# Optimization experiments

Hardware: AMD Instinct MI355X
Metric: run time of the kernel (lower is better)

Reference implementation:

```python
import jax, jax.numpy as jnp
import numpy as np

NEG = -1000000000.0

def _gat(x, adj_pos, W, a_src, a_dst):
    # x: [N,F], W: [H,F], a_src/a_dst: [1,H]
    h = x @ W.T                                          # [N,H]
    e = jax.nn.leaky_relu(h @ a_src.T + (h @ a_dst.T).T, 0.2)  # [N,N] additive attn
    e = jnp.where(adj_pos, e, NEG)
    alpha = jax.nn.softmax(e, axis=-1)
    return alpha @ h                                     # [N,H]

def setup_inputs() -> dict:
    key = jax.random.key(0)
    ks = jax.random.split(key, 24)
    N, F, Cf, C, H = 4096, 64, 10, 64, 128
    s = 0.05
    nrm = lambda k, shp: (jax.random.normal(k, shp, jnp.float32) * s)
    return dict(
        node_features=jax.random.normal(ks[0], (N, F), jnp.float32),
        candidate_features=jax.random.uniform(ks[1], (N, C, Cf), dtype=jnp.float32),
        adjacency=jax.random.randint(ks[2], (N, N), 0, 2).astype(jnp.int32),
        action_mask=jax.random.uniform(ks[3], (N, C), dtype=jnp.float32),
        W1=nrm(ks[4], (H, F)), a1s=nrm(ks[5], (1, H)), a1d=nrm(ks[6], (1, H)),
        W2=nrm(ks[7], (H, H)), a2s=nrm(ks[8], (1, H)), a2d=nrm(ks[9], (1, H)),
        ln_w=jnp.ones((H,), jnp.float32), ln_b=jnp.zeros((H,), jnp.float32),
        Wc1=nrm(ks[10], (H, Cf)), bc1=jnp.zeros((H,), jnp.float32),
        Wc2=nrm(ks[11], (H, H)), bc2=jnp.zeros((H,), jnp.float32),
        Wq=nrm(ks[12], (H, H)), bq=jnp.zeros((H,), jnp.float32),
        Ws1=nrm(ks[13], (H, 2 * H)), bs1=jnp.zeros((H,), jnp.float32),
        Ws2=nrm(ks[14], (1, H)), bs2=jnp.zeros((1,), jnp.float32),
    )

def reference(node_features, candidate_features, adjacency, action_mask,
              W1, a1s, a1d, W2, a2s, a2d, ln_w, ln_b,
              Wc1, bc1, Wc2, bc2, Wq, bq, Ws1, bs1, Ws2, bs2):
    gelu = lambda x: jax.nn.gelu(x, approximate=False)  # torch nn.GELU default (erf)
    adj_pos = adjacency > 0
    # two GAT layers with residual + LayerNorm
    h = jax.nn.relu(_gat(node_features, adj_pos, W1, a1s, a1d))      # [N,H]
    h = jax.nn.relu(_gat(h, adj_pos, W2, a2s, a2d)) + h
    mu = jnp.mean(h, axis=-1, keepdims=True)
    var = jnp.var(h, axis=-1, keepdims=True)
    h = (h - mu) * jax.lax.rsqrt(var + 1e-5) * ln_w + ln_b           # LayerNorm
    # candidate encoder
    cand = gelu(candidate_features @ Wc1.T + bc1)                    # [N,C,H]
    cand = gelu(cand @ Wc2.T + bc2)
    q = (h @ Wq.T + bq)[:, None, :]                                  # [N,1,H]
    fused = jnp.concatenate([q * cand, cand], axis=-1)               # [N,C,2H]
    logits = (gelu(fused @ Ws1.T + bs1) @ Ws2.T + bs2)[..., 0]       # [N,C]
    cf = candidate_features
    bias = (20.0 * cf[..., 0] + 4.0 * cf[..., 4] + 1.5 * cf[..., 5]
            + 1.5 * cf[..., 1] - 1.5 * cf[..., 2]
            + 1.2 * cf[..., 6] + 2.5 * cf[..., 7]
            + 1.6 * cf[..., 8] + 1.2 * cf[..., 9])
    logits = logits + bias
    # rows with no valid action: force action 0 valid
    no_valid = jnp.sum(action_mask, axis=-1) <= 0
    am = action_mask.at[:, 0].set(jnp.where(no_valid, 1.0, action_mask[:, 0]))
    return jnp.where(am > 0, logits, NEG)
```

## Files before the change

kernel.cpp:

```cpp
#include <hip/hip_runtime.h>
#include <hip/hip_bf16.h>
#include <math.h>

#define NN 4096
#define HD 128
#define NCAND 64
#define NCF 10
#define NSEG 16
#define NEGV (-1000000000.0f)

typedef __attribute__((ext_vector_type(8))) short short8_t;
typedef __attribute__((ext_vector_type(4))) float f32x4_t;

__device__ __forceinline__ short f2bf(float f) {
    union { __hip_bfloat16 h; short s; } v;
    v.h = __float2bfloat16(f);
    return v.s;
}
__device__ __forceinline__ float bf2f(short s) {
    union { unsigned u; float f; } v; v.u = ((unsigned)(unsigned short)s) << 16;
    return v.f;
}
__device__ __forceinline__ unsigned pk2(float a, float b) {
    union { __hip_bfloat162 h; unsigned u; } v;
    v.h = __float22bfloat162_rn(make_float2(a, b));
    return v.u;
}

__device__ __forceinline__ float gelu_f(float x) {
    float e = __builtin_amdgcn_exp2f(2.455466f * x);
    float r = __builtin_amdgcn_rcpf(e + 1.0f);
    return x - x * r;
}

__global__ __launch_bounds__(256) void prep_k(
    const int* __restrict__ adj, const float* __restrict__ Wc1,
    const float* __restrict__ Wc2, const float* __restrict__ Ws1,
    unsigned* __restrict__ adjb, short* __restrict__ Wc1b,
    short* __restrict__ Wc2b, short* __restrict__ Wfu)
{
    int tid = threadIdx.x;
    if (blockIdx.x < 2048) {
        long g = (long)blockIdx.x * 256 + tid;
        const int4* p = (const int4*)adj + g * 8;
        unsigned w = 0;
        #pragma unroll
        for (int e = 0; e < 8; ++e) {
            int4 v = p[e];
            w |= (unsigned)(v.x != 0) << (e*4 + 0);
            w |= (unsigned)(v.y != 0) << (e*4 + 1);
            w |= (unsigned)(v.z != 0) << (e*4 + 2);
            w |= (unsigned)(v.w != 0) << (e*4 + 3);
        }
        adjb[g] = w;
    } else {
        int g = (blockIdx.x - 2048) * 256 + tid;
        const int tot = 8 * 256;
        for (int e = g; e < 128*32; e += tot) {
            int t = e >> 5, k = e & 31;
            Wc1b[e] = (k < NCF) ? f2bf(Wc1[t*NCF + k]) : (short)0;
        }
        for (int e = g; e < 128*128; e += tot) {
            int h = e >> 7, pos = e & 127;
            int n = (pos >> 3) | ((pos & 7) << 4);
            Wc2b[e] = f2bf(Wc2[h*128 + n]);
        }
        for (int e = g; e < 128*256; e += tot) {
            int h = e >> 8, j = e & 255;
            int pos = j & 127;
            int n = (pos >> 3) | ((pos & 7) << 4);
            float v = (j < 128) ? Ws1[h*256 + 128 + n] : Ws1[h*256 + n];
            Wfu[e] = f2bf(v);
        }
    }
}

template<int K, int IN, int OUT>
__global__ __launch_bounds__(256) void gatin_k3(
    const float* __restrict__ in, const float* __restrict__ Wf,
    const float* __restrict__ nump, const float* __restrict__ denp,
    float* __restrict__ G1, const float* __restrict__ ln_w,
    const float* __restrict__ ln_b,
    const float* __restrict__ a_s, const float* __restrict__ a_d,
    float* __restrict__ sdv, short* __restrict__ Htb,
    const float* __restrict__ bias, float* __restrict__ outq)
{
    constexpr int AS = K + 4;
    __shared__ float in_s[16*AS];
    __shared__ float H_s[16*132];
    int tid = threadIdx.x;
    int n0 = blockIdx.x * 16;

    if (IN == 0) {
        constexpr int NV = 16*K/4;
        for (int idx = tid; idx < NV; idx += 256) {
            int row = idx / (K/4), c4 = idx - row*(K/4);
            *(float4*)&in_s[row*AS + c4*4] = *(const float4*)&in[(long)(n0+row)*K + c4*4];
        }
    } else {
        int row = tid >> 4, c8 = (tid & 15) * 8;
        float v[8];
        #pragma unroll
        for (int i = 0; i < 8; ++i) v[i] = 0.f;
        float den = 0.f;
        const float* npr = nump + (long)(n0 + row)*NSEG*HD + c8;
        const float* dpr = denp + (long)(n0 + row)*NSEG;
        #pragma unroll
        for (int s = 0; s < NSEG; ++s) {
            const float* np = npr + s*HD;
            float4 a0 = *(const float4*)np;
            float4 a1 = *(const float4*)(np + 4);
            v[0]+=a0.x; v[1]+=a0.y; v[2]+=a0.z; v[3]+=a0.w;
            v[4]+=a1.x; v[5]+=a1.y; v[6]+=a1.z; v[7]+=a1.w;
            den += dpr[s];
        }
        float rd = (den > 0.f) ? __builtin_amdgcn_rcpf(den) : 0.f;
        if (den > 0.f) rd = rd * (2.0f - den * rd);
        #pragma unroll
        for (int i = 0; i < 8; ++i) v[i] = fmaxf(v[i]*rd, 0.f);
        if (IN == 1) {
            float4 o0 = make_float4(v[0],v[1],v[2],v[3]);
            float4 o1 = make_float4(v[4],v[5],v[6],v[7]);
            *(float4*)&G1[(long)(n0+row)*HD + c8]     = o0;
            *(float4*)&G1[(long)(n0+row)*HD + c8 + 4] = o1;
        } else {
            const float* gp = G1 + (long)(n0+row)*HD + c8;
            float4 g0 = *(const float4*)gp;
            float4 g1 = *(const float4*)(gp + 4);
            v[0]+=g0.x; v[1]+=g0.y; v[2]+=g0.z; v[3]+=g0.w;
            v[4]+=g1.x; v[5]+=g1.y; v[6]+=g1.z; v[7]+=g1.w;
            float sm = 0.f, sq = 0.f;
            #pragma unroll
            for (int i = 0; i < 8; ++i) { sm += v[i]; sq += v[i]*v[i]; }
            sm += __shfl_xor(sm,1); sq += __shfl_xor(sq,1);
            sm += __shfl_xor(sm,2); sq += __shfl_xor(sq,2);
            sm += __shfl_xor(sm,4); sq += __shfl_xor(sq,4);
            sm += __shfl_xor(sm,8); sq += __shfl_xor(sq,8);
            float mu  = sm * (1.0f/128.0f);
            float var = sq * (1.0f/128.0f) - mu*mu;
            float nr  = rsqrtf(var + 1e-5f);
            float4 lw0 = *(const float4*)&ln_w[c8];
            float4 lw1 = *(const float4*)&ln_w[c8+4];
            float4 lb0 = *(const float4*)&ln_b[c8];
            float4 lb1 = *(const float4*)&ln_b[c8+4];
            v[0]=(v[0]-mu)*nr*lw0.x+lb0.x; v[1]=(v[1]-mu)*nr*lw0.y+lb0.y;
            v[2]=(v[2]-mu)*nr*lw0.z+lb0.z; v[3]=(v[3]-mu)*nr*lw0.w+lb0.w;
            v[4]=(v[4]-mu)*nr*lw1.x+lb1.x; v[5]=(v[5]-mu)*nr*lw1.y+lb1.y;
            v[6]=(v[6]-mu)*nr*lw1.z+lb1.z; v[7]=(v[7]-mu)*nr*lw1.w+lb1.w;
        }
        #pragma unroll
        for (int i = 0; i < 8; ++i) in_s[row*AS + c8 + i] = v[i];
    }
    __syncthreads();

    int w = tid >> 6, l = tid & 63, l15 = l & 15, qd = l >> 4;
    f32x4_t acc[2];
    acc[0] = (f32x4_t){0.f,0.f,0.f,0.f};
    acc[1] = (f32x4_t){0.f,0.f,0.f,0.f};
    #pragma unroll
    for (int kc = 0; kc < K/32; ++kc) {
        int k0 = kc*32 + qd*8;
        float4 x = *(const float4*)&in_s[l15*AS + k0];
        float4 y = *(const float4*)&in_s[l15*AS + k0 + 4];
        union { short8_t s; unsigned u[4]; } a;
        a.u[0]=pk2(x.x,x.y); a.u[1]=pk2(x.z,x.w);
        a.u[2]=pk2(y.x,y.y); a.u[3]=pk2(y.z,y.w);
        #pragma unroll
        for (int it = 0; it < 2; ++it) {
            int n = (w*2+it)*16 + l15;
            float4 w0 = *(const float4*)&Wf[(long)n*K + k0];
            float4 w1 = *(const float4*)&Wf[(long)n*K + k0 + 4];
            union { short8_t s; unsigned u[4]; } b;
            b.u[0]=pk2(w0.x,w0.y); b.u[1]=pk2(w0.z,w0.w);
            b.u[2]=pk2(w1.x,w1.y); b.u[3]=pk2(w1.z,w1.w);
            acc[it] = __builtin_amdgcn_mfma_f32_16x16x32_bf16(a.s, b.s, acc[it], 0,0,0);
        }
    }

    if (OUT == 1) {
        #pragma unroll
        for (int it = 0; it < 2; ++it) {
            int n = (w*2+it)*16 + l15;
            float bv = bias[n];
            #pragma unroll
            for (int r = 0; r < 4; ++r)
                outq[(long)(n0 + qd*4 + r)*HD + n] = acc[it][r] + bv;
        }
        return;
    }

    #pragma unroll
    for (int it = 0; it < 2; ++it)
        #pragma unroll
        for (int r = 0; r < 4; ++r)
            H_s[(qd*4+r)*132 + (w*2+it)*16 + l15] = acc[it][r];
    __syncthreads();
    {
        int row = tid >> 4, sg = tid & 15;
        int h0 = sg*8;
        float4 as0 = *(const float4*)&a_s[h0];
        float4 as1 = *(const float4*)&a_s[h0+4];
        float4 ad0 = *(const float4*)&a_d[h0];
        float4 ad1 = *(const float4*)&a_d[h0+4];
        float hv[8];
        #pragma unroll
        for (int e = 0; e < 8; ++e) hv[e] = H_s[row*132 + h0 + e];
        float sp = hv[0]*as0.x + hv[1]*as0.y + hv[2]*as0.z + hv[3]*as0.w
                 + hv[4]*as1.x + hv[5]*as1.y + hv[6]*as1.z + hv[7]*as1.w;
        float dp = hv[0]*ad0.x + hv[1]*ad0.y + hv[2]*ad0.z + hv[3]*ad0.w
                 + hv[4]*ad1.x + hv[5]*ad1.y + hv[6]*ad1.z + hv[7]*ad1.w;
        sp += __shfl_xor(sp,1); sp += __shfl_xor(sp,2);
        sp += __shfl_xor(sp,4); sp += __shfl_xor(sp,8);
        dp += __shfl_xor(dp,1); dp += __shfl_xor(dp,2);
        dp += __shfl_xor(dp,4); dp += __shfl_xor(dp,8);
        if (sg == 0) { sdv[n0+row] = sp; sdv[NN + n0 + row] = dp; }
    }
    {
        int h = tid & 127, pr = tid >> 7;
        unsigned u[4];
        #pragma unroll
        for (int c2 = 0; c2 < 4; ++c2)
            u[c2] = pk2(H_s[(pr*8 + 2*c2)*132 + h], H_s[(pr*8 + 2*c2 + 1)*132 + h]);
        *(uint4*)&Htb[(long)h*NN + n0 + pr*8] = make_uint4(u[0],u[1],u[2],u[3]);
    }
}

__global__ __launch_bounds__(256, 4) void agg_k5(
    const unsigned* __restrict__ adjb, const float* __restrict__ sdv,
    const short* __restrict__ Htb, float* __restrict__ num_part,
    float* __restrict__ den_part)
{
    __shared__ __align__(16) short Bs[128*72];
    __shared__ float dj_s[256];
    int tid = threadIdx.x;
    int i0 = blockIdx.x * 32;
    int seg = blockIdx.y;
    int w = tid >> 6, l = tid & 63, l15 = l & 15, qd = l >> 4;
    int mh = w >> 1, nh = w & 1;
    int arow = i0 + mh*16 + l15;
    float si = sdv[arow];
    const float C1 = 1.44269504f;
    const float C2 = 0.28853901f;

    dj_s[tid] = sdv[NN + seg*256 + tid];

    unsigned wbuf[8];
    {
        const uint4* ap = (const uint4*)&adjb[(long)arow*128 + seg*8];
        uint4 q0 = ap[0], q1 = ap[1];
        wbuf[0]=q0.x; wbuf[1]=q0.y; wbuf[2]=q0.z; wbuf[3]=q0.w;
        wbuf[4]=q1.x; wbuf[5]=q1.y; wbuf[6]=q1.z; wbuf[7]=q1.w;
    }

    int sh = tid >> 1, sj = (tid & 1) * 32;
    const short* srcb = Htb + (long)sh*NN + seg*256 + sj;

    f32x4_t acc[4];
    #pragma unroll
    for (int nt = 0; nt < 4; ++nt) acc[nt] = (f32x4_t){0.f,0.f,0.f,0.f};
    float den = 0.f;

    for (int c4 = 0; c4 < 4; ++c4) {
        __syncthreads();
        {
            const uint4* src = (const uint4*)(srcb + c4*64);
            uint4 v0 = src[0], v1 = src[1], v2 = src[2], v3 = src[3];
            uint4* dst = (uint4*)&Bs[sh*72 + sj];
            dst[0]=v0; dst[1]=v1; dst[2]=v2; dst[3]=v3;
        }
        __syncthreads();
        #pragma unroll
        for (int kc = 0; kc < 2; ++kc) {
            int jl = c4*64 + kc*32 + qd*8;
            float4 da = *(const float4*)&dj_s[jl];
            float4 db = *(const float4*)&dj_s[jl+4];
            unsigned byte_ = (wbuf[c4*2+kc] >> (qd*8)) & 0xffu;
            float dv[8] = {da.x,da.y,da.z,da.w,db.x,db.y,db.z,db.w};
            float v[8];
            #pragma unroll
            for (int e = 0; e < 8; ++e) {
                float z = si + dv[e];
                float k = (z > 0.f) ? C1 : C2;
                float wv = __builtin_amdgcn_exp2f(z * k);
                v[e] = ((byte_ >> e) & 1u) ? wv : 0.f;
                den += v[e];
            }
            union { short8_t s; unsigned u[4]; } a;
            a.u[0]=pk2(v[0],v[1]); a.u[1]=pk2(v[2],v[3]);
            a.u[2]=pk2(v[4],v[5]); a.u[3]=pk2(v[6],v[7]);
            int kb = kc*32 + qd*8;
            #pragma unroll
            for (int nt = 0; nt < 4; ++nt) {
                short8_t b = *(const short8_t*)&Bs[(nh*64 + nt*16 + l15)*72 + kb];
                acc[nt] = __builtin_amdgcn_mfma_f32_16x16x32_bf16(a.s, b, acc[nt], 0,0,0);
            }
        }
    }
    den += __shfl_xor(den, 16); den += __shfl_xor(den, 32);
    if (qd == 0 && nh == 0) den_part[(long)arow*NSEG + seg] = den;
    #pragma unroll
    for (int nt = 0; nt < 4; ++nt)
        #pragma unroll
        for (int r = 0; r < 4; ++r)
            num_part[((long)(i0 + mh*16 + qd*4 + r)*NSEG + seg)*HD
                     + nh*64 + nt*16 + l15] = acc[nt][r];
}

__device__ __forceinline__ short8_t mulq2(short8_t c, float4 qa, float4 qb) {
    union { short8_t s; unsigned u[4]; } r;
    r.u[0] = pk2(bf2f(c[0])*qa.x, bf2f(c[1])*qa.y);
    r.u[1] = pk2(bf2f(c[2])*qa.z, bf2f(c[3])*qa.w);
    r.u[2] = pk2(bf2f(c[4])*qb.x, bf2f(c[5])*qb.y);
    r.u[3] = pk2(bf2f(c[6])*qb.z, bf2f(c[7])*qb.w);
    return r.s;
}

__global__ __launch_bounds__(256, 4) void cand_k8(
    const float* __restrict__ cf, const float* __restrict__ am,
    const float* __restrict__ Qb,
    const short* __restrict__ Wc1b, const short* __restrict__ Wc2b,
    const short* __restrict__ Wfu,
    const float* __restrict__ bc1, const float* __restrict__ bc2,
    const float* __restrict__ bs1, const float* __restrict__ Ws2,
    const float* __restrict__ bs2, float* __restrict__ out)
{
    __shared__ __align__(16) short cand_s[128*136];
    __shared__ float bias_s[128];
    __shared__ __align__(16) float q_s[2][128];
    __shared__ float red_s[128*4];
    __shared__ float noval_s[2];
    int tid = threadIdx.x;
    long r0 = (long)blockIdx.x * 128;
    int w = tid >> 6, l = tid & 63, l15 = l & 15, qd = l >> 4;

    {
        float amv = am[r0 + (long)(w >> 1)*64 + l];
        float tot = amv;
        #pragma unroll
        for (int off = 32; off > 0; off >>= 1) tot += __shfl_xor(tot, off);
        if ((w & 1) == 0 && l == 0) noval_s[w >> 1] = (tot <= 0.f) ? 1.f : 0.f;
    }

    {
        int nd = tid >> 7, n = tid & 127;
        float qv = Qb[((r0 >> 6) + nd)*HD + n];
        int pos = ((n & 15) << 3) | (n >> 4);
        q_s[nd][pos] = qv;
    }

    {
        short8_t fa[2];
        #pragma unroll
        for (int im = 0; im < 2; ++im) {
            long row = r0 + (w*2+im)*16 + l15;
            union { short8_t s; unsigned u[4]; } a;
            float bp = 0.f;
            if (qd == 0) {
                float4 x = *(const float4*)&cf[row*10];
                float4 y = *(const float4*)&cf[row*10+4];
                a.u[0]=pk2(x.x,x.y); a.u[1]=pk2(x.z,x.w);
                a.u[2]=pk2(y.x,y.y); a.u[3]=pk2(y.z,y.w);
                bp = 20.0f*x.x + 1.5f*x.y - 1.5f*x.z + 4.0f*y.x
                   + 1.5f*y.y + 1.2f*y.z + 2.5f*y.w;
            } else if (qd == 1) {
                float2 x = *(const float2*)&cf[row*10+8];
                a.u[0]=pk2(x.x,x.y); a.u[1]=0; a.u[2]=0; a.u[3]=0;
                bp = 1.6f*x.x + 1.2f*x.y;
            } else { a.u[0]=a.u[1]=a.u[2]=a.u[3]=0; }
            bp += __shfl_xor(bp, 16);
            if (qd == 0) bias_s[(w*2+im)*16 + l15] = bp;
            fa[im] = a.s;
        }
        f32x4_t acc1[2][8];
        #pragma unroll
        for (int im = 0; im < 2; ++im)
            #pragma unroll
            for (int nt = 0; nt < 8; ++nt) acc1[im][nt] = (f32x4_t){0.f,0.f,0.f,0.f};
        #pragma unroll
        for (int nt = 0; nt < 8; ++nt) {
            short8_t b = *(const short8_t*)&Wc1b[(nt*16 + l15)*32 + qd*8];
            acc1[0][nt] = __builtin_amdgcn_mfma_f32_16x16x32_bf16(fa[0], b, acc1[0][nt], 0,0,0);
            acc1[1][nt] = __builtin_amdgcn_mfma_f32_16x16x32_bf16(fa[1], b, acc1[1][nt], 0,0,0);
        }
        float bv[8];
        #pragma unroll
        for (int nt = 0; nt < 8; ++nt) bv[nt] = bc1[nt*16 + l15];
        #pragma unroll
        for (int im = 0; im < 2; ++im)
            #pragma unroll
            for (int r = 0; r < 4; ++r) {
                unsigned u[4];
                #pragma unroll
                for (int ph = 0; ph < 4; ++ph) {
                    float g0 = gelu_f(acc1[im][2*ph][r]   + bv[2*ph]);
                    float g1 = gelu_f(acc1[im][2*ph+1][r] + bv[2*ph+1]);
                    u[ph] = pk2(g0, g1);
                }
                int m = (w*2+im)*16 + qd*4 + r;
                *(uint4*)&cand_s[m*136 + l15*8] = make_uint4(u[0],u[1],u[2],u[3]);
            }
    }
    __syncthreads();

    f32x4_t acc[8][2];
    #pragma unroll
    for (int mt = 0; mt < 8; ++mt) {
        acc[mt][0] = (f32x4_t){0.f,0.f,0.f,0.f};
        acc[mt][1] = (f32x4_t){0.f,0.f,0.f,0.f};
    }
    #pragma unroll
    for (int kc = 0; kc < 4; ++kc) {
        int kpos = kc*32 + qd*8;
        short8_t a[8];
        #pragma unroll
        for (int mt = 0; mt < 8; ++mt)
            a[mt] = *(const short8_t*)&cand_s[(mt*16 + l15)*136 + kpos];
        short8_t b0 = *(const short8_t*)&Wc2b[((w*2+0)*16 + l15)*128 + kpos];
        short8_t b1 = *(const short8_t*)&Wc2b[((w*2+1)*16 + l15)*128 + kpos];
        #pragma unroll
        for (int mt = 0; mt < 8; ++mt) {
            acc[mt][0] = __builtin_amdgcn_mfma_f32_16x16x32_bf16(a[mt], b0, acc[mt][0], 0,0,0);
            acc[mt][1] = __builtin_amdgcn_mfma_f32_16x16x32_bf16(a[mt], b1, acc[mt][1], 0,0,0);
        }
    }
    __syncthreads();

    {
        float bv0 = bc2[w*32 + l15];
        float bv1 = bc2[w*32 + 16 + l15];
        #pragma unroll
        for (int mt = 0; mt < 8; ++mt)
            #pragma unroll
            for (int r = 0; r < 4; ++r) {
                float g0 = gelu_f(acc[mt][0][r] + bv0);
                float g1 = gelu_f(acc[mt][1][r] + bv1);
                int m = mt*16 + qd*4 + r;
                *(unsigned*)&cand_s[m*136 + l15*8 + w*2] = pk2(g0, g1);
            }
    }
    __syncthreads();

    #pragma unroll
    for (int mt = 0; mt < 8; ++mt) {
        acc[mt][0] = (f32x4_t){0.f,0.f,0.f,0.f};
        acc[mt][1] = (f32x4_t){0.f,0.f,0.f,0.f};
    }
    #pragma unroll
    for (int kc = 0; kc < 4; ++kc) {
        int kpos = kc*32 + qd*8;
        short8_t a[8];
        #pragma unroll
        for (int mt = 0; mt < 8; ++mt)
            a[mt] = *(const short8_t*)&cand_s[(mt*16 + l15)*136 + kpos];
        short8_t b00 = *(const short8_t*)&Wfu[((w*2+0)*16 + l15)*256 + kpos];
        short8_t b10 = *(const short8_t*)&Wfu[((w*2+1)*16 + l15)*256 + kpos];
        short8_t b01 = *(const short8_t*)&Wfu[((w*2+0)*16 + l15)*256 + 128 + kpos];
        short8_t b11 = *(const short8_t*)&Wfu[((w*2+1)*16 + l15)*256 + 128 + kpos];
        float4 qa0 = *(const float4*)&q_s[0][kpos];
        float4 qb0 = *(const float4*)&q_s[0][kpos+4];
        float4 qa1 = *(const float4*)&q_s[1][kpos];
        float4 qb1 = *(const float4*)&q_s[1][kpos+4];
        short8_t b01q0 = mulq2(b01, qa0, qb0);
        short8_t b11q0 = mulq2(b11, qa0, qb0);
        short8_t b01q1 = mulq2(b01, qa1, qb1);
        short8_t b11q1 = mulq2(b11, qa1, qb1);
        #pragma unroll
        for (int mt = 0; mt < 8; ++mt) {
            short8_t bq0 = (mt < 4) ? b01q0 : b01q1;
            short8_t bq1 = (mt < 4) ? b11q0 : b11q1;
            acc[mt][0] = __builtin_amdgcn_mfma_f32_16x16x32_bf16(a[mt], b00, acc[mt][0], 0,0,0);
            acc[mt][1] = __builtin_amdgcn_mfma_f32_16x16x32_bf16(a[mt], b10, acc[mt][1], 0,0,0);
            acc[mt][0] = __builtin_amdgcn_mfma_f32_16x16x32_bf16(a[mt], bq0, acc[mt][0], 0,0,0);
            acc[mt][1] = __builtin_amdgcn_mfma_f32_16x16x32_bf16(a[mt], bq1, acc[mt][1], 0,0,0);
        }
    }

    {
        float bs1v0 = bs1[w*32 + l15],      bs1v1 = bs1[w*32 + 16 + l15];
        float ws2v0 = Ws2[w*32 + l15],      ws2v1 = Ws2[w*32 + 16 + l15];
        #pragma unroll
        for (int mt = 0; mt < 8; ++mt)
            #pragma unroll
            for (int r = 0; r < 4; ++r) {
                float p = gelu_f(acc[mt][0][r] + bs1v0) * ws2v0
                        + gelu_f(acc[mt][1][r] + bs1v1) * ws2v1;
                p += __shfl_xor(p,1); p += __shfl_xor(p,2);
                p += __shfl_xor(p,4); p += __shfl_xor(p,8);
                if (l15 == 0)
                    red_s[(mt*16 + qd*4 + r)*4 + w] = p;
            }
    }
    __syncthreads();

    if (tid < 128) {
        int m = tid;
        float lg = red_s[m*4] + red_s[m*4+1] + red_s[m*4+2] + red_s[m*4+3]
                 + bs2[0] + bias_s[m];
        float mk = am[r0 + m];
        if ((m & 63) == 0 && noval_s[m >> 6] > 0.f) mk = 1.0f;
        out[r0 + m] = (mk > 0.f) ? lg : NEGV;
    }
}

extern "C" void kernel_launch(void* const* d_in, const int* in_sizes, int n_in,
                              void* d_out, int out_size, void* d_ws, size_t ws_size,
                              hipStream_t stream)
{
    const float* X   = (const float*)d_in[0];
    const float* CF  = (const float*)d_in[1];
    const int*   ADJ = (const int*)d_in[2];
    const float* AM  = (const float*)d_in[3];
    const float* W1  = (const float*)d_in[4];
    const float* A1S = (const float*)d_in[5];
    const float* A1D = (const float*)d_in[6];
    const float* W2  = (const float*)d_in[7];
    const float* A2S = (const float*)d_in[8];
    const float* A2D = (const float*)d_in[9];
    const float* LNW = (const float*)d_in[10];
    const float* LNB = (const float*)d_in[11];
    const float* WC1 = (const float*)d_in[12];
    const float* BC1 = (const float*)d_in[13];
    const float* WC2 = (const float*)d_in[14];
    const float* BC2 = (const float*)d_in[15];
    const float* WQ  = (const float*)d_in[16];
    const float* BQ  = (const float*)d_in[17];
    const float* WS1 = (const float*)d_in[18];
    const float* BS1 = (const float*)d_in[19];
    const float* WS2 = (const float*)d_in[20];
    const float* BS2 = (const float*)d_in[21];
    float* OUT = (float*)d_out;

    float* ws = (float*)d_ws;
    float*    G1   = ws;
    float*    Qb   = ws + 524288;
    float*    sdv  = ws + 1048576;
    float*    denp = ws + 1056768;
    short*    Htb  = (short*)(ws + 1122304);
    unsigned* adjb = (unsigned*)(ws + 1384448);
    short*    Wc1b = (short*)(ws + 1908736);
    short*    Wc2b = (short*)(ws + 1910784);
    short*    Wfu  = (short*)(ws + 1918976);
    float*    nump = ws + 1935360;

    prep_k<<<2056, 256, 0, stream>>>(ADJ, WC1, WC2, WS1, adjb, Wc1b, Wc2b, Wfu);

    gatin_k3<64, 0, 0><<<256, 256, 0, stream>>>(
        X, W1, nullptr, nullptr, nullptr, nullptr, nullptr,
        A1S, A1D, sdv, Htb, nullptr, nullptr);
    agg_k5<<<dim3(128, NSEG), 256, 0, stream>>>(adjb, sdv, Htb, nump, denp);

    gatin_k3<128, 1, 0><<<256, 256, 0, stream>>>(
        nullptr, W2, nump, denp, G1, nullptr, nullptr,
        A2S, A2D, sdv, Htb, nullptr, nullptr);
    agg_k5<<<dim3(128, NSEG), 256, 0, stream>>>(adjb, sdv, Htb, nump, denp);

    gatin_k3<128, 2, 1><<<256, 256, 0, stream>>>(
        nullptr, WQ, nump, denp, G1, LNW, LNB,
        nullptr, nullptr, nullptr, nullptr, BQ, Qb);

    cand_k8<<<2048, 256, 0, stream>>>(CF, AM, Qb, Wc1b, Wc2b, Wfu,
                                      BC1, BC2, BS1, WS2, BS2, OUT);
}
```

Baseline: 270.3 us.

## Fuse first GAT projection into prep kernel and fold LN+Q projection into candidate kernel

Merges the layer-1 GAT input projection into the preprocessing launch as extra blocks, and moves the final aggregation, residual, LayerNorm and Wq projection into the candidate kernel, which each block now computes for its two nodes. This cuts two kernel launches and the Qb round trip through global memory. In exchange, each candidate block now does a scalar fp32 128x128 matvec and reads 16 partial segments per node. The serialized prologue before the main candidate MFMA work may add latency.

```diff
diff --git a/kernel.cpp b/kernel.cpp
--- a/kernel.cpp
+++ b/kernel.cpp
@@ -33,27 +33,36 @@
     return x - x * r;
 }
 
-__global__ __launch_bounds__(256) void prep_k(
+__global__ __launch_bounds__(256) void prep_gatin_k(
     const int* __restrict__ adj, const float* __restrict__ Wc1,
     const float* __restrict__ Wc2, const float* __restrict__ Ws1,
     unsigned* __restrict__ adjb, short* __restrict__ Wc1b,
-    short* __restrict__ Wc2b, short* __restrict__ Wfu)
+    short* __restrict__ Wc2b, short* __restrict__ Wfu,
+    const float* __restrict__ X, const float* __restrict__ W1,
+    const float* __restrict__ a_s, const float* __restrict__ a_d,
+    float* __restrict__ sdv, short* __restrict__ Htb)
 {
+    constexpr int K = 64, AS = 68;
+    __shared__ float in_s[16*AS];
+    __shared__ float H_s[16*132];
     int tid = threadIdx.x;
+
     if (blockIdx.x < 2048) {
         long g = (long)blockIdx.x * 256 + tid;
         const int4* p = (const int4*)adj + g * 8;
-        unsigned w = 0;
+        unsigned wd = 0;
         #pragma unroll
         for (int e = 0; e < 8; ++e) {
             int4 v = p[e];
-            w |= (unsigned)(v.x != 0) << (e*4 + 0);
-            w |= (unsigned)(v.y != 0) << (e*4 + 1);
-            w |= (unsigned)(v.z != 0) << (e*4 + 2);
-            w |= (unsigned)(v.w != 0) << (e*4 + 3);
-        }
-        adjb[g] = w;
-    } else {
+            wd |= (unsigned)(v.x != 0) << (e*4 + 0);
+            wd |= (unsigned)(v.y != 0) << (e*4 + 1);
+            wd |= (unsigned)(v.z != 0) << (e*4 + 2);
+            wd |= (unsigned)(v.w != 0) << (e*4 + 3);
+        }
+        adjb[g] = wd;
+        return;
+    }
+    if (blockIdx.x < 2056) {
         int g = (blockIdx.x - 2048) * 256 + tid;
         const int tot = 8 * 256;
         for (int e = g; e < 128*32; e += tot) {
@@ -72,6 +81,75 @@
             float v = (j < 128) ? Ws1[h*256 + 128 + n] : Ws1[h*256 + n];
             Wfu[e] = f2bf(v);
         }
+        return;
+    }
+
+    int n0 = (blockIdx.x - 2056) * 16;
+    {
+        constexpr int NV = 16*K/4;
+        for (int idx = tid; idx < NV; idx += 256) {
+            int row = idx / (K/4), c4 = idx - row*(K/4);
+            *(float4*)&in_s[row*AS + c4*4] = *(const float4*)&X[(long)(n0+row)*K + c4*4];
+        }
+    }
+    __syncthreads();
+
+    int w = tid >> 6, l = tid & 63, l15 = l & 15, qd = l >> 4;
+    f32x4_t acc[2];
+    acc[0] = (f32x4_t){0.f,0.f,0.f,0.f};
+    acc[1] = (f32x4_t){0.f,0.f,0.f,0.f};
+    #pragma unroll
+    for (int kc = 0; kc < K/32; ++kc) {
+        int k0 = kc*32 + qd*8;
+        float4 x = *(const float4*)&in_s[l15*AS + k0];
+        float4 y = *(const float4*)&in_s[l15*AS + k0 + 4];
+        union { short8_t s; unsigned u[4]; } a;
+        a.u[0]=pk2(x.x,x.y); a.u[1]=pk2(x.z,x.w);
+        a.u[2]=pk2(y.x,y.y); a.u[3]=pk2(y.z,y.w);
+        #pragma unroll
+        for (int it = 0; it < 2; ++it) {
+            int n = (w*2+it)*16 + l15;
+            float4 w0 = *(const float4*)&W1[(long)n*K + k0];
+            float4 w1 = *(const float4*)&W1[(long)n*K + k0 + 4];
+            union { short8_t s; unsigned u[4]; } b;
+            b.u[0]=pk2(w0.x,w0.y); b.u[1]=pk2(w0.z,w0.w);
+            b.u[2]=pk2(w1.x,w1.y); b.u[3]=pk2(w1.z,w1.w);
+            acc[it] = __builtin_amdgcn_mfma_f32_16x16x32_bf16(a.s, b.s, acc[it], 0,0,0);
+        }
+    }
+    #pragma unroll
+    for (int it = 0; it < 2; ++it)
+        #pragma unroll
+        for (int r = 0; r < 4; ++r)
+            H_s[(qd*4+r)*132 + (w*2+it)*16 + l15] = acc[it][r];
+    __syncthreads();
+    {
+        int row = tid >> 4, sg = tid & 15;
+        int h0 = sg*8;
+        float4 as0 = *(const float4*)&a_s[h0];
+        float4 as1 = *(const float4*)&a_s[h0+4];
+        float4 ad0 = *(const float4*)&a_d[h0];
+        float4 ad1 = *(const float4*)&a_d[h0+4];
+        float hv[8];
+        #pragma unroll
+        for (int e = 0; e < 8; ++e) hv[e] = H_s[row*132 + h0 + e];
+        float sp = hv[0]*as0.x + hv[1]*as0.y + hv[2]*as0.z + hv[3]*as0.w
+                 + hv[4]*as1.x + hv[5]*as1.y + hv[6]*as1.z + hv[7]*as1.w;
+        float dp = hv[0]*ad0.x + hv[1]*ad0.y + hv[2]*ad0.z + hv[3]*ad0.w
+                 + hv[4]*ad1.x + hv[5]*ad1.y + hv[6]*ad1.z + hv[7]*ad1.w;
+        sp += __shfl_xor(sp,1); sp += __shfl_xor(sp,2);
+        sp += __shfl_xor(sp,4); sp += __shfl_xor(sp,8);
+        dp += __shfl_xor(dp,1); dp += __shfl_xor(dp,2);
+        dp += __shfl_xor(dp,4); dp += __shfl_xor(dp,8);
+        if (sg == 0) { sdv[n0+row] = sp; sdv[NN + n0 + row] = dp; }
+    }
+    {
+        int h = tid & 127, pr = tid >> 7;
+        unsigned u[4];
+        #pragma unroll
+        for (int c2 = 0; c2 < 4; ++c2)
+            u[c2] = pk2(H_s[(pr*8 + 2*c2)*132 + h], H_s[(pr*8 + 2*c2 + 1)*132 + h]);
+        *(uint4*)&Htb[(long)h*NN + n0 + pr*8] = make_uint4(u[0],u[1],u[2],u[3]);
     }
 }
 
@@ -123,30 +201,6 @@
             float4 o1 = make_float4(v[4],v[5],v[6],v[7]);
             *(float4*)&G1[(long)(n0+row)*HD + c8]     = o0;
             *(float4*)&G1[(long)(n0+row)*HD + c8 + 4] = o1;
-        } else {
-            const float* gp = G1 + (long)(n0+row)*HD + c8;
-            float4 g0 = *(const float4*)gp;
-            float4 g1 = *(const float4*)(gp + 4);
-            v[0]+=g0.x; v[1]+=g0.y; v[2]+=g0.z; v[3]+=g0.w;
-            v[4]+=g1.x; v[5]+=g1.y; v[6]+=g1.z; v[7]+=g1.w;
-            float sm = 0.f, sq = 0.f;
-            #pragma unroll
-            for (int i = 0; i < 8; ++i) { sm += v[i]; sq += v[i]*v[i]; }
-            sm += __shfl_xor(sm,1); sq += __shfl_xor(sq,1);
-            sm += __shfl_xor(sm,2); sq += __shfl_xor(sq,2);
-            sm += __shfl_xor(sm,4); sq += __shfl_xor(sq,4);
-            sm += __shfl_xor(sm,8); sq += __shfl_xor(sq,8);
-            float mu  = sm * (1.0f/128.0f);
-            float var = sq * (1.0f/128.0f) - mu*mu;
-            float nr  = rsqrtf(var + 1e-5f);
-            float4 lw0 = *(const float4*)&ln_w[c8];
-            float4 lw1 = *(const float4*)&ln_w[c8+4];
-            float4 lb0 = *(const float4*)&ln_b[c8];
-            float4 lb1 = *(const float4*)&ln_b[c8+4];
-            v[0]=(v[0]-mu)*nr*lw0.x+lb0.x; v[1]=(v[1]-mu)*nr*lw0.y+lb0.y;
-            v[2]=(v[2]-mu)*nr*lw0.z+lb0.z; v[3]=(v[3]-mu)*nr*lw0.w+lb0.w;
-            v[4]=(v[4]-mu)*nr*lw1.x+lb1.x; v[5]=(v[5]-mu)*nr*lw1.y+lb1.y;
-            v[6]=(v[6]-mu)*nr*lw1.z+lb1.z; v[7]=(v[7]-mu)*nr*lw1.w+lb1.w;
         }
         #pragma unroll
         for (int i = 0; i < 8; ++i) in_s[row*AS + c8 + i] = v[i];
@@ -175,18 +229,6 @@
             b.u[2]=pk2(w1.x,w1.y); b.u[3]=pk2(w1.z,w1.w);
             acc[it] = __builtin_amdgcn_mfma_f32_16x16x32_bf16(a.s, b.s, acc[it], 0,0,0);
         }
-    }
-
-    if (OUT == 1) {
-        #pragma unroll
-        for (int it = 0; it < 2; ++it) {
-            int n = (w*2+it)*16 + l15;
-            float bv = bias[n];
-            #pragma unroll
-            for (int r = 0; r < 4; ++r)
-                outq[(long)(n0 + qd*4 + r)*HD + n] = acc[it][r] + bv;
-        }
-        return;
     }
 
     #pragma unroll
@@ -315,9 +357,12 @@
     return r.s;
 }
 
-__global__ __launch_bounds__(256, 4) void cand_k8(
+__global__ __launch_bounds__(256, 4) void cand_k9(
     const float* __restrict__ cf, const float* __restrict__ am,
-    const float* __restrict__ Qb,
+    const float* __restrict__ nump, const float* __restrict__ denp,
+    const float* __restrict__ G1, const float* __restrict__ ln_w,
+    const float* __restrict__ ln_b, const float* __restrict__ Wq,
+    const float* __restrict__ bq,
     const short* __restrict__ Wc1b, const short* __restrict__ Wc2b,
     const short* __restrict__ Wfu,
     const float* __restrict__ bc1, const float* __restrict__ bc2,
@@ -329,6 +374,7 @@
     __shared__ __align__(16) float q_s[2][128];
     __shared__ float red_s[128*4];
     __shared__ float noval_s[2];
+    __shared__ float hln_s[2][128];
     int tid = threadIdx.x;
     long r0 = (long)blockIdx.x * 128;
     int w = tid >> 6, l = tid & 63, l15 = l & 15, qd = l >> 4;
@@ -341,11 +387,50 @@
         if ((w & 1) == 0 && l == 0) noval_s[w >> 1] = (tot <= 0.f) ? 1.f : 0.f;
     }
 
-    {
-        int nd = tid >> 7, n = tid & 127;
-        float qv = Qb[((r0 >> 6) + nd)*HD + n];
+    if (w < 2) {
+        int node = (int)(r0 >> 6) + w;
+        float v0 = 0.f, v1 = 0.f, den = 0.f;
+        const float* np = nump + (long)node*NSEG*HD;
+        const float* dp = denp + (long)node*NSEG;
+        #pragma unroll
+        for (int s = 0; s < NSEG; ++s) {
+            v0 += np[s*HD + l];
+            v1 += np[s*HD + l + 64];
+            den += dp[s];
+        }
+        float rd = (den > 0.f) ? __builtin_amdgcn_rcpf(den) : 0.f;
+        if (den > 0.f) rd = rd * (2.0f - den * rd);
+        v0 = fmaxf(v0*rd, 0.f) + G1[(long)node*HD + l];
+        v1 = fmaxf(v1*rd, 0.f) + G1[(long)node*HD + l + 64];
+        float sm = v0 + v1, sq = v0*v0 + v1*v1;
+        #pragma unroll
+        for (int off = 32; off > 0; off >>= 1) {
+            sm += __shfl_xor(sm, off);
+            sq += __shfl_xor(sq, off);
+        }
+        float mu  = sm * (1.0f/128.0f);
+        float var = sq * (1.0f/128.0f) - mu*mu;
+        float nr  = rsqrtf(var + 1e-5f);
+        hln_s[w][l]      = (v0 - mu)*nr*ln_w[l]      + ln_b[l];
+        hln_s[w][l + 64] = (v1 - mu)*nr*ln_w[l + 64] + ln_b[l + 64];
+    }
+    __syncthreads();
+
+    if (tid < 128) {
+        int n = tid;
+        const float* wq = Wq + (long)n*HD;
+        const float* h0 = hln_s[0];
+        const float* h1 = hln_s[1];
+        float a0 = bq[n], a1 = a0;
+        #pragma unroll 8
+        for (int k = 0; k < 128; k += 4) {
+            float4 wv = *(const float4*)&wq[k];
+            a0 += h0[k]*wv.x + h0[k+1]*wv.y + h0[k+2]*wv.z + h0[k+3]*wv.w;
+            a1 += h1[k]*wv.x + h1[k+1]*wv.y + h1[k+2]*wv.z + h1[k+3]*wv.w;
+        }
         int pos = ((n & 15) << 3) | (n >> 4);
-        q_s[nd][pos] = qv;
+        q_s[0][pos] = a0;
+        q_s[1][pos] = a1;
     }
 
     {
@@ -532,32 +617,24 @@
 
     float* ws = (float*)d_ws;
     float*    G1   = ws;
-    float*    Qb   = ws + 524288;
-    float*    sdv  = ws + 1048576;
-    float*    denp = ws + 1056768;
-    short*    Htb  = (short*)(ws + 1122304);
-    unsigned* adjb = (unsigned*)(ws + 1384448);
-    short*    Wc1b = (short*)(ws + 1908736);
-    short*    Wc2b = (short*)(ws + 1910784);
-    short*    Wfu  = (short*)(ws + 1918976);
-    float*    nump = ws + 1935360;
-
-    prep_k<<<2056, 256, 0, stream>>>(ADJ, WC1, WC2, WS1, adjb, Wc1b, Wc2b, Wfu);
-
-    gatin_k3<64, 0, 0><<<256, 256, 0, stream>>>(
-        X, W1, nullptr, nullptr, nullptr, nullptr, nullptr,
-        A1S, A1D, sdv, Htb, nullptr, nullptr);
+    float*    sdv  = ws + 524288;
+    float*    denp = ws + 532480;
+    short*    Htb  = (short*)(ws + 598016);
+    unsigned* adjb = (unsigned*)(ws + 860160);
+    short*    Wc1b = (short*)(ws + 1384448);
+    short*    Wc2b = (short*)(ws + 1386496);
+    short*    Wfu  = (short*)(ws + 1394688);
+    float*    nump = ws + 1411072;
+
+    prep_gatin_k<<<2312, 256, 0, stream>>>(ADJ, WC1, WC2, WS1,
+                                           adjb, Wc1b, Wc2b, Wfu,
+                                           X, W1, A1S, A1D, sdv, Htb);
     agg_k5<<<dim3(128, NSEG), 256, 0, stream>>>(adjb, sdv, Htb, nump, denp);
-
     gatin_k3<128, 1, 0><<<256, 256, 0, stream>>>(
         nullptr, W2, nump, denp, G1, nullptr, nullptr,
         A2S, A2D, sdv, Htb, nullptr, nullptr);
     agg_k5<<<dim3(128, NSEG), 256, 0, stream>>>(adjb, sdv, Htb, nump, denp);
-
-    gatin_k3<128, 2, 1><<<256, 256, 0, stream>>>(
-        nullptr, WQ, nump, denp, G1, LNW, LNB,
-        nullptr, nullptr, nullptr, nullptr, BQ, Qb);
-
-    cand_k8<<<2048, 256, 0, stream>>>(CF, AM, Qb, Wc1b, Wc2b, Wfu,
-                                      BC1, BC2, BS1, WS2, BS2, OUT);
-}
+    cand_k9<<<2048, 256, 0, stream>>>(CF, AM, nump, denp, G1, LNW, LNB, WQ, BQ,
+                                      Wc1b, Wc2b, Wfu, BC1, BC2, BS1, WS2, BS2,
+                                      OUT);
+}
```

Result: no change. 274.3 us (+1.5%).
